# Kernel optimization log

Hardware: AMD Instinct MI355X
Metric: run time of the kernel (lower is better)

The kernel has to match this reference:

```python
import jax, jax.numpy as jnp
import numpy as np

jax.config.update("jax_enable_x64", True)  # torch lfilter runs in double precision

SR = 24000
RES_SIZE = 64
R_MIN, R_MAX = 0.9999, 0.99999
B, T = 4, 120000


def setup_inputs() -> dict:
    # Probe coefficients (fixed buffers, computed exactly as in Probe.__init__)
    theta_min = 2 * np.pi * 10.0 / SR
    theta_max = 2 * np.pi * 100.0 / SR
    theta = np.exp(np.linspace(np.log(theta_min), np.log(theta_max), RES_SIZE))
    radii = np.linspace(R_MIN, R_MAX, RES_SIZE)
    a1 = -2.0 * radii * np.cos(theta)          # [C]
    a2 = radii ** 2                             # [C]
    b0 = (1.0 - radii) * 0.5                    # [C]

    # Tank mixing weight: orthogonal init, shape [out=64, in=128] (rows orthonormal)
    rng = np.random.default_rng(1337)
    q, _ = np.linalg.qr(rng.standard_normal((2 * RES_SIZE, RES_SIZE)))  # [128,64], orthonormal cols
    W = q.T.astype(np.float32)                  # [64,128]

    key = jax.random.key(0)
    k1, k2 = jax.random.split(key)
    pred = jax.random.normal(k1, (B, 1, T), dtype=jnp.float32)
    target = jax.random.normal(k2, (B, 1, T), dtype=jnp.float32)
    return {
        "pred": pred,
        "target": target,
        "a1": jnp.asarray(a1, jnp.float64),
        "a2": jnp.asarray(a2, jnp.float64),
        "b0": jnp.asarray(b0, jnp.float64),
        "W": jnp.asarray(W, jnp.float32),
    }


def _biquad_bank(x, a1, a2, b0):
    """Biquad filter bank. x: [N, T] float64; coeffs: [C]. Returns [N, C, T].
    y[t] = b0*x[t] - a1*y[t-1] - a2*y[t-2]  (a0 = 1, b1 = b2 = 0, clamp=False)
    """
    n = x.shape[0]
    c = a1.shape[0]

    def step(carry, xt):
        y1, y2 = carry  # each [N, C]
        y = b0[None, :] * xt[:, None] - a1[None, :] * y1 - a2[None, :] * y2
        return (y, y1), y

    init = (jnp.zeros((n, c), x.dtype), jnp.zeros((n, c), x.dtype))
    _, ys = jax.lax.scan(step, init, x.T)      # [T, N, C]
    return jnp.transpose(ys, (1, 2, 0))        # [N, C, T]


def _probe(x, a1, a2, b0):
    """x: [B,1,T] float -> [B, 2C, T] float32 (fwd state ++ bwd state)."""
    xs = x[:, 0, :].astype(jnp.float64)        # [B, T]
    # run forward-time and reversed-time filters in one batched scan
    both = jnp.concatenate([xs, xs[:, ::-1]], axis=0)       # [2B, T]
    ys = _biquad_bank(both, a1, a2, b0)                      # [2B, C, T]
    nb = xs.shape[0]
    fwd_state = ys[:nb]                                      # [B, C, T]
    bwd_state = ys[nb:][:, :, ::-1]                          # [B, C, T] (flipped back)
    return jnp.concatenate([fwd_state, bwd_state], axis=1).astype(jnp.float32)


def _tank(x, W):
    """x: [B, 2C, T], W: [C, 2C] -> tanh(W @ x): [B, C, T]."""
    return jnp.tanh(jnp.einsum("bct,oc->bot", x, W))


def reference(pred, target, a1, a2, b0, W):
    t = pred.shape[-1]
    margin = t // 3
    p_emb = _tank(_probe(pred, a1, a2, b0), W)    # [B, C, T]
    t_emb = _tank(_probe(target, a1, a2, b0), W)  # [B, C, T]
    p_valid = p_emb[..., margin:t - margin]
    t_valid = t_emb[..., margin:t - margin]
    return jnp.mean(jnp.abs(p_valid - t_valid))
```

## Files before the change

kernel.cpp:

```cpp
#include <hip/hip_runtime.h>

#define T_LEN 120000
#define LBLK 160
#define PBLK 750
#define SEG_LEN 25
#define NSEG 30
#define CCH 32
#define NCHUNK (LBLK / CCH)
#define BATCH 4
#define K0 250
#define NKV 250
#define DENOM 20480000.0
#define YSTR 130

typedef _Float16 half8 __attribute__((ext_vector_type(8)));
typedef float f32x4 __attribute__((ext_vector_type(4)));

__device__ __forceinline__ float fast_tanh(float x) {
  float e = __expf(2.0f * x);
  return 1.0f - 2.0f / (e + 1.0f);
}

__device__ __forceinline__ bool coeffs_are_f64(const void* a2p) {
  double probe = *(const double*)a2p;
  return probe > 0.9 && probe < 1.0;
}
__device__ __forceinline__ double coeff_d(const void* p, bool f64, int ch) {
  return f64 ? ((const double*)p)[ch] : (double)((const float*)p)[ch];
}

__device__ __forceinline__ void mat_pow(double A1, double A2, int e,
                                        double& r00, double& r01,
                                        double& r10, double& r11) {
  double m00 = -A1, m01 = -A2, m10 = 1.0, m11 = 0.0;
  r00 = 1.0; r01 = 0.0; r10 = 0.0; r11 = 1.0;
  while (e) {
    if (e & 1) {
      double t00 = r00 * m00 + r01 * m10, t01 = r00 * m01 + r01 * m11;
      double t10 = r10 * m00 + r11 * m10, t11 = r10 * m01 + r11 * m11;
      r00 = t00; r01 = t01; r10 = t10; r11 = t11;
    }
    e >>= 1;
    if (e) {
      double t00 = m00 * m00 + m01 * m10, t01 = m00 * m01 + m01 * m11;
      double t10 = m10 * m00 + m11 * m10, t11 = m10 * m01 + m11 * m11;
      m00 = t00; m01 = t01; m10 = t10; m11 = t11;
    }
  }
}

__global__ __launch_bounds__(64) void pass1(
    const float* __restrict__ pred, const float* __restrict__ tgt,
    const void* a1p, const void* a2p, const void* b0p,
    double* __restrict__ fbuf)
{
  int k = blockIdx.x, r = blockIdx.y;
  int i = r >> 3, d = (r >> 2) & 1, b = r & 3;
  const float* sig = (i ? tgt : pred) + b * T_LEN;
  __shared__ float xs[LBLK];
  int base = k * LBLK;
  for (int j = threadIdx.x; j < LBLK; j += 64)
    xs[j] = d ? sig[T_LEN - 1 - (base + j)] : sig[base + j];
  __syncthreads();
  int ch = threadIdx.x;
  bool f64 = coeffs_are_f64(a2p);
  float A1 = (float)coeff_d(a1p, f64, ch);
  float A2 = (float)coeff_d(a2p, f64, ch);
  float B0 = (float)coeff_d(b0p, f64, ch);
  float y1 = 0.0f, y2 = 0.0f;
  for (int j = 0; j < LBLK; ++j) {
    float y = fmaf(-A1, y1, fmaf(-A2, y2, B0 * xs[j]));
    y2 = y1; y1 = y;
  }
  int s = r * 64 + ch;
  ((double2*)fbuf)[(size_t)k * 1024 + s] = make_double2((double)y1, (double)y2);
}

__global__ __launch_bounds__(64) void pass2a(
    const void* a1p, const void* a2p,
    const double* __restrict__ fbuf, double* __restrict__ sbuf)
{
  int seg = blockIdx.x >> 4;
  int s = ((blockIdx.x & 15) << 6) + threadIdx.x;
  int ch = s & 63;
  bool f64 = coeffs_are_f64(a2p);
  double r00, r01, r10, r11;
  mat_pow(coeff_d(a1p, f64, ch), coeff_d(a2p, f64, ch), LBLK, r00, r01, r10, r11);
  const double2* fb = (const double2*)fbuf;
  double y1 = 0.0, y2 = 0.0;
  for (int jj = 0; jj < SEG_LEN / 5; ++jj) {
    size_t kb = (size_t)(seg * SEG_LEN + jj * 5) * 1024 + s;
    double2 f0 = fb[kb], f1 = fb[kb + 1024], f2 = fb[kb + 2048],
            f3 = fb[kb + 3072], f4 = fb[kb + 4096];
    double n1, n2;
    n1 = r00*y1 + r01*y2 + f0.x; n2 = r10*y1 + r11*y2 + f0.y; y1=n1; y2=n2;
    n1 = r00*y1 + r01*y2 + f1.x; n2 = r10*y1 + r11*y2 + f1.y; y1=n1; y2=n2;
    n1 = r00*y1 + r01*y2 + f2.x; n2 = r10*y1 + r11*y2 + f2.y; y1=n1; y2=n2;
    n1 = r00*y1 + r01*y2 + f3.x; n2 = r10*y1 + r11*y2 + f3.y; y1=n1; y2=n2;
    n1 = r00*y1 + r01*y2 + f4.x; n2 = r10*y1 + r11*y2 + f4.y; y1=n1; y2=n2;
  }
  ((double2*)sbuf)[(size_t)seg * 1024 + s] = make_double2(y1, y2);
}

__global__ __launch_bounds__(256) void pass2b(
    const void* a1p, const void* a2p,
    const double* __restrict__ sbuf, double* __restrict__ tbuf)
{
  int s = blockIdx.x * 256 + threadIdx.x;
  int ch = s & 63;
  bool f64 = coeffs_are_f64(a2p);
  double r00, r01, r10, r11;
  mat_pow(coeff_d(a1p, f64, ch), coeff_d(a2p, f64, ch), LBLK * SEG_LEN,
          r00, r01, r10, r11);
  const double2* sb = (const double2*)sbuf;
  double2* tb = (double2*)tbuf;
  double y1 = 0.0, y2 = 0.0;
  #pragma unroll 1
  for (int half = 0; half < 2; ++half) {
    int base = half * 15;
    double2 f[15];
    #pragma unroll
    for (int q = 0; q < 15; ++q) f[q] = sb[(size_t)(base + q) * 1024 + s];
    #pragma unroll
    for (int q = 0; q < 15; ++q) {
      tb[(size_t)(base + q) * 1024 + s] = make_double2(y1, y2);
      double n1 = r00 * y1 + r01 * y2 + f[q].x;
      double n2 = r10 * y1 + r11 * y2 + f[q].y;
      y1 = n1; y2 = n2;
    }
  }
}

__global__ __launch_bounds__(256, 4) void pass3(
    const float* __restrict__ pred, const float* __restrict__ tgt,
    const void* a1p, const void* a2p, const void* b0p,
    const float* __restrict__ W, const double* __restrict__ fbuf,
    const double* __restrict__ tbuf, double* __restrict__ wsum)
{
  int k = K0 + blockIdx.x;
  int b = blockIdx.y;
  int tid = threadIdx.x;
  __shared__ __align__(16) _Float16 ys[2][64 * YSTR];
  __shared__ float red[4];

  int g = tid >> 6, lane = tid & 63;
  int gu = __builtin_amdgcn_readfirstlane(g);
  int iu = gu >> 1, du = gu & 1;
  int ch = lane;
  int n0 = gu * 16;
  int lm = lane & 15, quad = lane >> 4;

  bool f64 = coeffs_are_f64(a2p);
  double A1d = coeff_d(a1p, f64, ch), A2d = coeff_d(a2p, f64, ch);
  double B0d = coeff_d(b0p, f64, ch);
  float A1 = (float)A1d, A2 = (float)A2d, B0 = (float)B0d;
  float IA2 = (float)(1.0 / A2d);

  int m = du ? (PBLK - k) : k;
  int seg = m / SEG_LEN, j = m - seg * SEG_LEN;
  int s = (iu * 8 + du * 4 + b) * 64 + ch;
  double r00, r01, r10, r11;
  mat_pow(A1d, A2d, LBLK, r00, r01, r10, r11);
  double2 v0 = ((const double2*)tbuf)[(size_t)seg * 1024 + s];
  double y1 = v0.x, y2 = v0.y;
  const double2* fb = (const double2*)fbuf + (size_t)(seg * SEG_LEN) * 1024 + s;
  #pragma unroll 1
  for (int bb = 0; bb < 24; bb += 8) {
    double2 f[8];
    #pragma unroll
    for (int q = 0; q < 8; ++q) f[q] = fb[(size_t)(bb + q) * 1024];
    #pragma unroll
    for (int q = 0; q < 8; ++q) {
      if (bb + q < j) {
        double n1 = r00 * y1 + r01 * y2 + f[q].x;
        double n2 = r10 * y1 + r11 * y2 + f[q].y;
        y1 = n1; y2 = n2;
      }
    }
  }
  float st0 = (float)y1, st1 = (float)y2;

  half8 wf[4][4];
  #pragma unroll
  for (int m0 = 0; m0 < 4; ++m0) {
    #pragma unroll
    for (int k0 = 0; k0 < 4; ++k0) {
      const float* wp = W + (m0 * 16 + lm) * 128 + k0 * 32 + quad * 8;
      float4 wa = *(const float4*)wp, wb = *(const float4*)(wp + 4);
      half8 h;
      h[0] = (_Float16)wa.x; h[1] = (_Float16)wa.y;
      h[2] = (_Float16)wa.z; h[3] = (_Float16)wa.w;
      h[4] = (_Float16)wb.x; h[5] = (_Float16)wb.y;
      h[6] = (_Float16)wb.z; h[7] = (_Float16)wb.w;
      wf[m0][k0] = h;
    }
  }

  const float* xp = (iu ? tgt : pred) + b * T_LEN + k * LBLK;

  float loss = 0.0f;
  for (int cc = 0; cc < NCHUNK; ++cc) {
    _Float16* yb = ys[cc & 1];
    if (du == 0) {
      #pragma unroll
      for (int tt = 0; tt < CCH; ++tt) {
        float x = xp[cc * CCH + tt];
        float y = fmaf(-A1, st0, fmaf(-A2, st1, B0 * x));
        yb[(2 * tt + iu) * YSTR + ch] = (_Float16)y;
        st1 = st0; st0 = y;
      }
    } else {
      #pragma unroll
      for (int tt = 0; tt < CCH; ++tt) {
        float x = xp[cc * CCH + tt];
        yb[(2 * tt + iu) * YSTR + 64 + ch] = (_Float16)st0;
        float ym2 = (fmaf(-A1, st1, B0 * x) - st0) * IA2;
        st0 = st1; st1 = ym2;
      }
    }
    __syncthreads();

    const _Float16* yrow = &yb[(n0 + lm) * YSTR + quad * 8];
    half8 bf0 = *(const half8*)(yrow);
    half8 bf1 = *(const half8*)(yrow + 32);
    half8 bf2 = *(const half8*)(yrow + 64);
    half8 bf3 = *(const half8*)(yrow + 96);
    #pragma unroll
    for (int m0 = 0; m0 < 4; ++m0) {
      f32x4 c = {0.f, 0.f, 0.f, 0.f};
      c = __builtin_amdgcn_mfma_f32_16x16x32_f16(wf[m0][0], bf0, c, 0, 0, 0);
      c = __builtin_amdgcn_mfma_f32_16x16x32_f16(wf[m0][1], bf1, c, 0, 0, 0);
      c = __builtin_amdgcn_mfma_f32_16x16x32_f16(wf[m0][2], bf2, c, 0, 0, 0);
      c = __builtin_amdgcn_mfma_f32_16x16x32_f16(wf[m0][3], bf3, c, 0, 0, 0);
      #pragma unroll
      for (int r = 0; r < 4; ++r) {
        float vv = fast_tanh(c[r]);
        float p = __shfl_xor(vv, 1);
        loss += fabsf(vv - p);
      }
    }
  }

  #pragma unroll
  for (int off = 32; off > 0; off >>= 1) loss += __shfl_down(loss, off);
  if ((tid & 63) == 0) red[tid >> 6] = loss;
  __syncthreads();
  if (tid == 0) atomicAdd(wsum, (double)(red[0] + red[1] + red[2] + red[3]));
}

__global__ void finalize(const double* __restrict__ wsum, float* __restrict__ out) {
  out[0] = (float)(wsum[0] / DENOM);
}

extern "C" void kernel_launch(void* const* d_in, const int* in_sizes, int n_in,
                              void* d_out, int out_size, void* d_ws, size_t ws_size,
                              hipStream_t stream) {
  const float* pred = (const float*)d_in[0];
  const float* tgt  = (const float*)d_in[1];
  const void* a1p = d_in[2];
  const void* a2p = d_in[3];
  const void* b0p = d_in[4];
  const float* W  = (const float*)d_in[5];
  float* out = (float*)d_out;

  double* base = (double*)d_ws;
  double* wsum = base;
  double* fbuf = base + 8;
  double* sbuf = fbuf + (size_t)PBLK * 1024 * 2;
  double* tbuf = sbuf + (size_t)NSEG * 1024 * 2;

  hipMemsetAsync(wsum, 0, sizeof(double), stream);
  pass1<<<dim3(PBLK, 16), 64, 0, stream>>>(pred, tgt, a1p, a2p, b0p, fbuf);
  pass2a<<<NSEG * 16, 64, 0, stream>>>(a1p, a2p, fbuf, sbuf);
  pass2b<<<dim3(4), 256, 0, stream>>>(a1p, a2p, sbuf, tbuf);
  pass3<<<dim3(NKV, BATCH), 256, 0, stream>>>(pred, tgt, a1p, a2p, b0p,
                                              W, fbuf, tbuf, wsum);
  finalize<<<1, 1, 0, stream>>>(wsum, out);
}
```

Before: 127.8 us.

## Split middle blocks into halves with precomputed states and drop unused prefix blocks

```diff
diff --git a/kernel.cpp b/kernel.cpp
--- a/kernel.cpp
+++ b/kernel.cpp
@@ -2,11 +2,15 @@
 
 #define T_LEN 120000
 #define LBLK 160
+#define HBLK 80
 #define PBLK 750
+#define PB_USED 500
 #define SEG_LEN 25
-#define NSEG 30
-#define CCH 32
-#define NCHUNK (LBLK / CCH)
+#define NSEG_USED 20
+#define SEGC0 10
+#define NSEGC 11
+#define CCH 16
+#define NCHUNK 5
 #define BATCH 4
 #define K0 250
 #define NKV 250
@@ -52,8 +56,13 @@
 __global__ __launch_bounds__(64) void pass1(
     const float* __restrict__ pred, const float* __restrict__ tgt,
     const void* a1p, const void* a2p, const void* b0p,
-    double* __restrict__ fbuf)
-{
+    double* __restrict__ fbuf, double* __restrict__ fmid,
+    double* __restrict__ wsum)
+{
+  if ((blockIdx.x | blockIdx.y) == 0 && threadIdx.x == 0) {
+    wsum[0] = 0.0;
+    ((unsigned int*)(wsum + 1))[0] = 0u;
+  }
   int k = blockIdx.x, r = blockIdx.y;
   int i = r >> 3, d = (r >> 2) & 1, b = r & 3;
   const float* sig = (i ? tgt : pred) + b * T_LEN;
@@ -68,11 +77,18 @@
   float A2 = (float)coeff_d(a2p, f64, ch);
   float B0 = (float)coeff_d(b0p, f64, ch);
   float y1 = 0.0f, y2 = 0.0f;
-  for (int j = 0; j < LBLK; ++j) {
+  for (int j = 0; j < HBLK; ++j) {
     float y = fmaf(-A1, y1, fmaf(-A2, y2, B0 * xs[j]));
     y2 = y1; y1 = y;
   }
   int s = r * 64 + ch;
+  if (k >= K0 && k < K0 + NKV)
+    ((double2*)fmid)[(size_t)(k - K0) * 1024 + s] =
+        make_double2((double)y1, (double)y2);
+  for (int j = HBLK; j < LBLK; ++j) {
+    float y = fmaf(-A1, y1, fmaf(-A2, y2, B0 * xs[j]));
+    y2 = y1; y1 = y;
+  }
   ((double2*)fbuf)[(size_t)k * 1024 + s] = make_double2((double)y1, (double)y2);
 }
 
@@ -117,37 +133,86 @@
   double y1 = 0.0, y2 = 0.0;
   #pragma unroll 1
   for (int half = 0; half < 2; ++half) {
-    int base = half * 15;
-    double2 f[15];
-    #pragma unroll
-    for (int q = 0; q < 15; ++q) f[q] = sb[(size_t)(base + q) * 1024 + s];
-    #pragma unroll
-    for (int q = 0; q < 15; ++q) {
-      tb[(size_t)(base + q) * 1024 + s] = make_double2(y1, y2);
+    int bse = half * 10;
+    double2 f[10];
+    #pragma unroll
+    for (int q = 0; q < 10; ++q) f[q] = sb[(size_t)(bse + q) * 1024 + s];
+    #pragma unroll
+    for (int q = 0; q < 10; ++q) {
+      tb[(size_t)(bse + q) * 1024 + s] = make_double2(y1, y2);
       double n1 = r00 * y1 + r01 * y2 + f[q].x;
       double n2 = r10 * y1 + r11 * y2 + f[q].y;
       y1 = n1; y2 = n2;
     }
   }
-}
-
-__global__ __launch_bounds__(256, 4) void pass3(
+  tb[(size_t)NSEG_USED * 1024 + s] = make_double2(y1, y2);
+}
+
+__global__ __launch_bounds__(64) void pass2c(
+    const void* a1p, const void* a2p,
+    const double* __restrict__ fbuf, const double* __restrict__ fmid,
+    const double* __restrict__ tbuf, double* __restrict__ stbuf)
+{
+  int seg = SEGC0 + (blockIdx.x >> 4);
+  int s = ((blockIdx.x & 15) << 6) + threadIdx.x;
+  int ch = s & 63;
+  bool f64 = coeffs_are_f64(a2p);
+  double A1d = coeff_d(a1p, f64, ch), A2d = coeff_d(a2p, f64, ch);
+  double p00, p01, p10, p11;
+  mat_pow(A1d, A2d, HBLK, p00, p01, p10, p11);
+  double r00 = p00*p00 + p01*p10, r01 = p00*p01 + p01*p11;
+  double r10 = p10*p00 + p11*p10, r11 = p10*p01 + p11*p11;
+  double2 v0 = ((const double2*)tbuf)[(size_t)seg * 1024 + s];
+  double y1 = v0.x, y2 = v0.y;
+  const double2* fb = (const double2*)fbuf;
+  const double2* fm = (const double2*)fmid;
+  double2* st = (double2*)stbuf;
+  #pragma unroll 1
+  for (int jb = 0; jb < SEG_LEN; jb += 5) {
+    double2 fv[5], fmv[5];
+    #pragma unroll
+    for (int q = 0; q < 5; ++q) {
+      int m = seg * SEG_LEN + jb + q;
+      int mc = m < PB_USED ? m : PB_USED - 1;
+      fv[q]  = fb[(size_t)mc * 1024 + s];
+      fmv[q] = fm[(size_t)(mc - K0) * 1024 + s];
+    }
+    #pragma unroll
+    for (int q = 0; q < 5; ++q) {
+      int m = seg * SEG_LEN + jb + q;
+      if (m <= K0 + NKV) {
+        int mi = m - K0;
+        st[(size_t)(mi * 2) * 1024 + s] = make_double2(y1, y2);
+        if (m < K0 + NKV) {
+          st[(size_t)(mi * 2 + 1) * 1024 + s] =
+              make_double2(p00 * y1 + p01 * y2 + fmv[q].x,
+                           p10 * y1 + p11 * y2 + fmv[q].y);
+          double n1 = r00 * y1 + r01 * y2 + fv[q].x;
+          double n2 = r10 * y1 + r11 * y2 + fv[q].y;
+          y1 = n1; y2 = n2;
+        }
+      }
+    }
+  }
+}
+
+__global__ __launch_bounds__(512, 8) void pass3(
     const float* __restrict__ pred, const float* __restrict__ tgt,
     const void* a1p, const void* a2p, const void* b0p,
-    const float* __restrict__ W, const double* __restrict__ fbuf,
-    const double* __restrict__ tbuf, double* __restrict__ wsum)
+    const float* __restrict__ W, const double* __restrict__ stbuf,
+    double* __restrict__ wsum, float* __restrict__ out)
 {
   int k = K0 + blockIdx.x;
   int b = blockIdx.y;
   int tid = threadIdx.x;
   __shared__ __align__(16) _Float16 ys[2][64 * YSTR];
-  __shared__ float red[4];
+  __shared__ float red[8];
 
   int g = tid >> 6, lane = tid & 63;
   int gu = __builtin_amdgcn_readfirstlane(g);
-  int iu = gu >> 1, du = gu & 1;
+  int iu = gu & 1, du = (gu >> 1) & 1, hu = gu >> 2;
+  int mh = gu >> 2, cg = gu & 3;
   int ch = lane;
-  int n0 = gu * 16;
   int lm = lane & 15, quad = lane >> 4;
 
   bool f64 = coeffs_are_f64(a2p);
@@ -156,47 +221,31 @@
   float A1 = (float)A1d, A2 = (float)A2d, B0 = (float)B0d;
   float IA2 = (float)(1.0 / A2d);
 
-  int m = du ? (PBLK - k) : k;
-  int seg = m / SEG_LEN, j = m - seg * SEG_LEN;
+  int m = PBLK - k;
+  int sb_blk = du ? (hu ? (m - 1) : m) : k;
   int s = (iu * 8 + du * 4 + b) * 64 + ch;
-  double r00, r01, r10, r11;
-  mat_pow(A1d, A2d, LBLK, r00, r01, r10, r11);
-  double2 v0 = ((const double2*)tbuf)[(size_t)seg * 1024 + s];
-  double y1 = v0.x, y2 = v0.y;
-  const double2* fb = (const double2*)fbuf + (size_t)(seg * SEG_LEN) * 1024 + s;
-  #pragma unroll 1
-  for (int bb = 0; bb < 24; bb += 8) {
-    double2 f[8];
-    #pragma unroll
-    for (int q = 0; q < 8; ++q) f[q] = fb[(size_t)(bb + q) * 1024];
-    #pragma unroll
-    for (int q = 0; q < 8; ++q) {
-      if (bb + q < j) {
-        double n1 = r00 * y1 + r01 * y2 + f[q].x;
-        double n2 = r10 * y1 + r11 * y2 + f[q].y;
-        y1 = n1; y2 = n2;
-      }
-    }
-  }
-  float st0 = (float)y1, st1 = (float)y2;
-
-  half8 wf[4][4];
+  double2 v0 =
+      ((const double2*)stbuf)[(size_t)((sb_blk - K0) * 2 + hu) * 1024 + s];
+  float st0 = (float)v0.x, st1 = (float)v0.y;
+
+  half8 wf[2][4];
   #pragma unroll
-  for (int m0 = 0; m0 < 4; ++m0) {
+  for (int mm = 0; mm < 2; ++mm) {
     #pragma unroll
     for (int k0 = 0; k0 < 4; ++k0) {
-      const float* wp = W + (m0 * 16 + lm) * 128 + k0 * 32 + quad * 8;
+      const float* wp = W + ((mh * 2 + mm) * 16 + lm) * 128 + k0 * 32 + quad * 8;
       float4 wa = *(const float4*)wp, wb = *(const float4*)(wp + 4);
       half8 h;
       h[0] = (_Float16)wa.x; h[1] = (_Float16)wa.y;
       h[2] = (_Float16)wa.z; h[3] = (_Float16)wa.w;
       h[4] = (_Float16)wb.x; h[5] = (_Float16)wb.y;
       h[6] = (_Float16)wb.z; h[7] = (_Float16)wb.w;
-      wf[m0][k0] = h;
-    }
-  }
-
-  const float* xp = (iu ? tgt : pred) + b * T_LEN + k * LBLK;
+      wf[mm][k0] = h;
+    }
+  }
+
+  const float* xp = (iu ? tgt : pred) + b * T_LEN + k * LBLK + hu * HBLK;
+  int cb = hu * 32 + iu;
 
   float loss = 0.0f;
   for (int cc = 0; cc < NCHUNK; ++cc) {
@@ -206,32 +255,32 @@
       for (int tt = 0; tt < CCH; ++tt) {
         float x = xp[cc * CCH + tt];
         float y = fmaf(-A1, st0, fmaf(-A2, st1, B0 * x));
-        yb[(2 * tt + iu) * YSTR + ch] = (_Float16)y;
+        yb[(cb + 2 * tt) * YSTR + ch] = (_Float16)y;
         st1 = st0; st0 = y;
       }
     } else {
       #pragma unroll
       for (int tt = 0; tt < CCH; ++tt) {
         float x = xp[cc * CCH + tt];
-        yb[(2 * tt + iu) * YSTR + 64 + ch] = (_Float16)st0;
+        yb[(cb + 2 * tt) * YSTR + 64 + ch] = (_Float16)st0;
         float ym2 = (fmaf(-A1, st1, B0 * x) - st0) * IA2;
         st0 = st1; st1 = ym2;
       }
     }
     __syncthreads();
 
-    const _Float16* yrow = &yb[(n0 + lm) * YSTR + quad * 8];
+    const _Float16* yrow = &yb[(cg * 16 + lm) * YSTR + quad * 8];
     half8 bf0 = *(const half8*)(yrow);
     half8 bf1 = *(const half8*)(yrow + 32);
     half8 bf2 = *(const half8*)(yrow + 64);
     half8 bf3 = *(const half8*)(yrow + 96);
     #pragma unroll
-    for (int m0 = 0; m0 < 4; ++m0) {
+    for (int mm = 0; mm < 2; ++mm) {
       f32x4 c = {0.f, 0.f, 0.f, 0.f};
-      c = __builtin_amdgcn_mfma_f32_16x16x32_f16(wf[m0][0], bf0, c, 0, 0, 0);
-      c = __builtin_amdgcn_mfma_f32_16x16x32_f16(wf[m0][1], bf1, c, 0, 0, 0);
-      c = __builtin_amdgcn_mfma_f32_16x16x32_f16(wf[m0][2], bf2, c, 0, 0, 0);
-      c = __builtin_amdgcn_mfma_f32_16x16x32_f16(wf[m0][3], bf3, c, 0, 0, 0);
+      c = __builtin_amdgcn_mfma_f32_16x16x32_f16(wf[mm][0], bf0, c, 0, 0, 0);
+      c = __builtin_amdgcn_mfma_f32_16x16x32_f16(wf[mm][1], bf1, c, 0, 0, 0);
+      c = __builtin_amdgcn_mfma_f32_16x16x32_f16(wf[mm][2], bf2, c, 0, 0, 0);
+      c = __builtin_amdgcn_mfma_f32_16x16x32_f16(wf[mm][3], bf3, c, 0, 0, 0);
       #pragma unroll
       for (int r = 0; r < 4; ++r) {
         float vv = fast_tanh(c[r]);
@@ -243,13 +292,20 @@
 
   #pragma unroll
   for (int off = 32; off > 0; off >>= 1) loss += __shfl_down(loss, off);
-  if ((tid & 63) == 0) red[tid >> 6] = loss;
+  if (lane == 0) red[g] = loss;
   __syncthreads();
-  if (tid == 0) atomicAdd(wsum, (double)(red[0] + red[1] + red[2] + red[3]));
-}
-
-__global__ void finalize(const double* __restrict__ wsum, float* __restrict__ out) {
-  out[0] = (float)(wsum[0] / DENOM);
+  if (tid == 0) {
+    float blk = ((red[0] + red[1]) + (red[2] + red[3])) +
+                ((red[4] + red[5]) + (red[6] + red[7]));
+    atomicAdd(wsum, (double)blk);
+    __threadfence();
+    unsigned int n = atomicAdd((unsigned int*)(wsum + 1), 1u);
+    if (n == (unsigned int)(NKV * BATCH - 1)) {
+      __threadfence();
+      double tot = atomicAdd(wsum, 0.0);
+      out[0] = (float)(tot / DENOM);
+    }
+  }
 }
 
 extern "C" void kernel_launch(void* const* d_in, const int* in_sizes, int n_in,
@@ -266,14 +322,16 @@
   double* base = (double*)d_ws;
   double* wsum = base;
   double* fbuf = base + 8;
-  double* sbuf = fbuf + (size_t)PBLK * 1024 * 2;
-  double* tbuf = sbuf + (size_t)NSEG * 1024 * 2;
-
-  hipMemsetAsync(wsum, 0, sizeof(double), stream);
-  pass1<<<dim3(PBLK, 16), 64, 0, stream>>>(pred, tgt, a1p, a2p, b0p, fbuf);
-  pass2a<<<NSEG * 16, 64, 0, stream>>>(a1p, a2p, fbuf, sbuf);
+  double* fmid = fbuf + (size_t)PB_USED * 1024 * 2;
+  double* sbuf = fmid + (size_t)NKV * 1024 * 2;
+  double* tbuf = sbuf + (size_t)32 * 1024 * 2;
+  double* stbuf = tbuf + (size_t)32 * 1024 * 2;
+
+  pass1<<<dim3(PB_USED, 16), 64, 0, stream>>>(pred, tgt, a1p, a2p, b0p,
+                                              fbuf, fmid, wsum);
+  pass2a<<<NSEG_USED * 16, 64, 0, stream>>>(a1p, a2p, fbuf, sbuf);
   pass2b<<<dim3(4), 256, 0, stream>>>(a1p, a2p, sbuf, tbuf);
-  pass3<<<dim3(NKV, BATCH), 256, 0, stream>>>(pred, tgt, a1p, a2p, b0p,
-                                              W, fbuf, tbuf, wsum);
-  finalize<<<1, 1, 0, stream>>>(wsum, out);
-}
+  pass2c<<<NSEGC * 16, 64, 0, stream>>>(a1p, a2p, fbuf, fmid, tbuf, stbuf);
+  pass3<<<dim3(NKV, BATCH), 512, 0, stream>>>(pred, tgt, a1p, a2p, b0p,
+                                              W, stbuf, wsum, out);
+}
```

New measurement: 142.5 us. 1.11x slower.

## Trim unused prefix blocks, fold segment scan into pass3, drop memset/finalize launches

Applied to the files above, without the earlier changes.

```diff
diff --git a/kernel.cpp b/kernel.cpp
--- a/kernel.cpp
+++ b/kernel.cpp
@@ -3,10 +3,11 @@
 #define T_LEN 120000
 #define LBLK 160
 #define PBLK 750
+#define PB_USED 500
 #define SEG_LEN 25
-#define NSEG 30
+#define NSEG_USED 20
 #define CCH 32
-#define NCHUNK (LBLK / CCH)
+#define NCHUNK 5
 #define BATCH 4
 #define K0 250
 #define NKV 250
@@ -52,8 +53,12 @@
 __global__ __launch_bounds__(64) void pass1(
     const float* __restrict__ pred, const float* __restrict__ tgt,
     const void* a1p, const void* a2p, const void* b0p,
-    double* __restrict__ fbuf)
+    double* __restrict__ fbuf, double* __restrict__ wsum)
 {
+  if ((blockIdx.x | blockIdx.y) == 0 && threadIdx.x == 0) {
+    wsum[0] = 0.0;
+    ((unsigned int*)(wsum + 1))[0] = 0u;
+  }
   int k = blockIdx.x, r = blockIdx.y;
   int i = r >> 3, d = (r >> 2) & 1, b = r & 3;
   const float* sig = (i ? tgt : pred) + b * T_LEN;
@@ -102,40 +107,12 @@
   ((double2*)sbuf)[(size_t)seg * 1024 + s] = make_double2(y1, y2);
 }
 
-__global__ __launch_bounds__(256) void pass2b(
-    const void* a1p, const void* a2p,
-    const double* __restrict__ sbuf, double* __restrict__ tbuf)
-{
-  int s = blockIdx.x * 256 + threadIdx.x;
-  int ch = s & 63;
-  bool f64 = coeffs_are_f64(a2p);
-  double r00, r01, r10, r11;
-  mat_pow(coeff_d(a1p, f64, ch), coeff_d(a2p, f64, ch), LBLK * SEG_LEN,
-          r00, r01, r10, r11);
-  const double2* sb = (const double2*)sbuf;
-  double2* tb = (double2*)tbuf;
-  double y1 = 0.0, y2 = 0.0;
-  #pragma unroll 1
-  for (int half = 0; half < 2; ++half) {
-    int base = half * 15;
-    double2 f[15];
-    #pragma unroll
-    for (int q = 0; q < 15; ++q) f[q] = sb[(size_t)(base + q) * 1024 + s];
-    #pragma unroll
-    for (int q = 0; q < 15; ++q) {
-      tb[(size_t)(base + q) * 1024 + s] = make_double2(y1, y2);
-      double n1 = r00 * y1 + r01 * y2 + f[q].x;
-      double n2 = r10 * y1 + r11 * y2 + f[q].y;
-      y1 = n1; y2 = n2;
-    }
-  }
-}
-
 __global__ __launch_bounds__(256, 4) void pass3(
     const float* __restrict__ pred, const float* __restrict__ tgt,
     const void* a1p, const void* a2p, const void* b0p,
     const float* __restrict__ W, const double* __restrict__ fbuf,
-    const double* __restrict__ tbuf, double* __restrict__ wsum)
+    const double* __restrict__ sbuf, double* __restrict__ wsum,
+    float* __restrict__ out)
 {
   int k = K0 + blockIdx.x;
   int b = blockIdx.y;
@@ -159,16 +136,38 @@
   int m = du ? (PBLK - k) : k;
   int seg = m / SEG_LEN, j = m - seg * SEG_LEN;
   int s = (iu * 8 + du * 4 + b) * 64 + ch;
+
+  double q00, q01, q10, q11;
+  mat_pow(A1d, A2d, LBLK * SEG_LEN, q00, q01, q10, q11);
+  double y1 = 0.0, y2 = 0.0;
+  const double2* sb = (const double2*)sbuf;
+  #pragma unroll 1
+  for (int qq = 0; qq < NSEG_USED; qq += 5) {
+    double2 f[5];
+    #pragma unroll
+    for (int p = 0; p < 5; ++p) f[p] = sb[(size_t)(qq + p) * 1024 + s];
+    #pragma unroll
+    for (int p = 0; p < 5; ++p) {
+      if (qq + p < seg) {
+        double n1 = q00 * y1 + q01 * y2 + f[p].x;
+        double n2 = q10 * y1 + q11 * y2 + f[p].y;
+        y1 = n1; y2 = n2;
+      }
+    }
+  }
+
   double r00, r01, r10, r11;
   mat_pow(A1d, A2d, LBLK, r00, r01, r10, r11);
-  double2 v0 = ((const double2*)tbuf)[(size_t)seg * 1024 + s];
-  double y1 = v0.x, y2 = v0.y;
-  const double2* fb = (const double2*)fbuf + (size_t)(seg * SEG_LEN) * 1024 + s;
+  const double2* fb = (const double2*)fbuf;
   #pragma unroll 1
   for (int bb = 0; bb < 24; bb += 8) {
     double2 f[8];
     #pragma unroll
-    for (int q = 0; q < 8; ++q) f[q] = fb[(size_t)(bb + q) * 1024];
+    for (int q = 0; q < 8; ++q) {
+      int blk = seg * SEG_LEN + bb + q;
+      if (blk >= PB_USED) blk = PB_USED - 1;
+      f[q] = fb[(size_t)blk * 1024 + s];
+    }
     #pragma unroll
     for (int q = 0; q < 8; ++q) {
       if (bb + q < j) {
@@ -243,13 +242,19 @@
 
   #pragma unroll
   for (int off = 32; off > 0; off >>= 1) loss += __shfl_down(loss, off);
-  if ((tid & 63) == 0) red[tid >> 6] = loss;
+  if (lane == 0) red[g] = loss;
   __syncthreads();
-  if (tid == 0) atomicAdd(wsum, (double)(red[0] + red[1] + red[2] + red[3]));
-}
-
-__global__ void finalize(const double* __restrict__ wsum, float* __restrict__ out) {
-  out[0] = (float)(wsum[0] / DENOM);
+  if (tid == 0) {
+    float blk = (red[0] + red[1]) + (red[2] + red[3]);
+    atomicAdd(wsum, (double)blk);
+    __threadfence();
+    unsigned int n = atomicAdd((unsigned int*)(wsum + 1), 1u);
+    if (n == (unsigned int)(NKV * BATCH - 1)) {
+      __threadfence();
+      double tot = atomicAdd(wsum, 0.0);
+      out[0] = (float)(tot / DENOM);
+    }
+  }
 }
 
 extern "C" void kernel_launch(void* const* d_in, const int* in_sizes, int n_in,
@@ -266,14 +271,11 @@
   double* base = (double*)d_ws;
   double* wsum = base;
   double* fbuf = base + 8;
-  double* sbuf = fbuf + (size_t)PBLK * 1024 * 2;
-  double* tbuf = sbuf + (size_t)NSEG * 1024 * 2;
-
-  hipMemsetAsync(wsum, 0, sizeof(double), stream);
-  pass1<<<dim3(PBLK, 16), 64, 0, stream>>>(pred, tgt, a1p, a2p, b0p, fbuf);
-  pass2a<<<NSEG * 16, 64, 0, stream>>>(a1p, a2p, fbuf, sbuf);
-  pass2b<<<dim3(4), 256, 0, stream>>>(a1p, a2p, sbuf, tbuf);
+  double* sbuf = fbuf + (size_t)PB_USED * 1024 * 2;
+
+  pass1<<<dim3(PB_USED, 16), 64, 0, stream>>>(pred, tgt, a1p, a2p, b0p,
+                                              fbuf, wsum);
+  pass2a<<<NSEG_USED * 16, 64, 0, stream>>>(a1p, a2p, fbuf, sbuf);
   pass3<<<dim3(NKV, BATCH), 256, 0, stream>>>(pred, tgt, a1p, a2p, b0p,
-                                              W, fbuf, tbuf, wsum);
-  finalize<<<1, 1, 0, stream>>>(wsum, out);
-}
+                                              W, fbuf, sbuf, wsum, out);
+}
```

New measurement: 126.9 us. Within noise of the previous version (-0.8%).
